# Performance work log

Measured on AMD Instinct MI355X. Metric: run time of the kernel, lower is better.

The kernel has to match this reference:

```python
import jax, jax.numpy as jnp
import numpy as np

N = 100000          # nodes
E = 1600000         # edges (before self-loops)
F_IN = 256          # num_node_features
F_MID = F_IN // 2   # conv1 out = 128
HID = 128           # hidden_channels
OUT = 64            # num_label_features
G = 128             # num graphs in batch
NEG_SLOPE = 0.2


def setup_inputs() -> dict:
    key = jax.random.key(0)
    ks = jax.random.split(key, 16)
    s = 0.05
    return {
        "x": jax.random.normal(ks[0], (N, F_IN), dtype=jnp.float32),
        "edge_index": jax.random.randint(ks[1], (2, E), 0, N, dtype=jnp.int64),
        "batch": jnp.sort(jax.random.randint(ks[2], (N,), 0, G, dtype=jnp.int64)),
        # GATConv 1 (heads=1)
        "W1": jax.random.normal(ks[3], (F_IN, F_MID), jnp.float32) * s,
        "a1_src": jax.random.normal(ks[4], (F_MID,), jnp.float32) * s,
        "a1_dst": jax.random.normal(ks[5], (F_MID,), jnp.float32) * s,
        "b1": jnp.zeros((F_MID,), jnp.float32),
        # GATConv 2
        "W2": jax.random.normal(ks[6], (F_MID, HID), jnp.float32) * s,
        "a2_src": jax.random.normal(ks[7], (HID,), jnp.float32) * s,
        "a2_dst": jax.random.normal(ks[8], (HID,), jnp.float32) * s,
        "b2": jnp.zeros((HID,), jnp.float32),
        # GlobalAttention gate nn
        "gate_W": jax.random.normal(ks[9], (HID, 1), jnp.float32) * s,
        "gate_b": jnp.zeros((1,), jnp.float32),
        # final linear
        "lin_W": jax.random.normal(ks[10], (HID, OUT), jnp.float32) * s,
        "lin_b": jnp.zeros((OUT,), jnp.float32),
    }


def _gat_conv(x, edge_index, W, a_src, a_dst, bias):
    """PyG GATConv, heads=1, add_self_loops=True, negative_slope=0.2."""
    n = x.shape[0]
    h = x @ W                                   # [N, F]
    loop = jnp.arange(n, dtype=edge_index.dtype)
    src = jnp.concatenate([edge_index[0], loop])  # message sources j
    dst = jnp.concatenate([edge_index[1], loop])  # aggregation targets i
    # per-node attention logits, gathered per-edge
    al = (h @ a_src)[src] + (h @ a_dst)[dst]    # [E+N]
    al = jax.nn.leaky_relu(al, NEG_SLOPE)
    # segment softmax over incoming edges of each dst node
    m = jax.ops.segment_max(al, dst, num_segments=n)
    e = jnp.exp(al - m[dst])
    s = jax.ops.segment_sum(e, dst, num_segments=n)
    coef = e / (s[dst] + 1e-16)
    out = jax.ops.segment_sum(h[src] * coef[:, None], dst, num_segments=n)
    return out + bias


def reference(x, edge_index, batch, W1, a1_src, a1_dst, b1,
              W2, a2_src, a2_dst, b2, gate_W, gate_b, lin_W, lin_b):
    h = _gat_conv(x, edge_index, W1, a1_src, a1_dst, b1)
    h = jax.nn.relu(h)
    h = _gat_conv(h, edge_index, W2, a2_src, a2_dst, b2)
    # GlobalAttention pooling: segment softmax of gate over batch ids
    gate = (h @ gate_W + gate_b)[:, 0]          # [N]
    gm = jax.ops.segment_max(gate, batch, num_segments=G)
    ge = jnp.exp(gate - gm[batch])
    gs = jax.ops.segment_sum(ge, batch, num_segments=G)
    attn = ge / (gs[batch] + 1e-16)
    pooled = jax.ops.segment_sum(h * attn[:, None], batch, num_segments=G)  # [G, HID]
    pooled = jax.nn.relu(pooled)
    # dropout p=0.5 is identity at inference
    return pooled @ lin_W + lin_b               # [G, OUT]
```

## Files before the change

kernel.cpp:

```cpp
#include <hip/hip_runtime.h>
#include <hip/hip_bf16.h>
#include <math.h>

#define NNODES 100000
#define NEDGES 1600000
#define EN     1700000
#define F_IN   256
#define F_MID  128
#define HID    128
#define NG     128
#define NOUT   64
#define SCAN_CHUNK 2048
#define NCHUNK ((NNODES + SCAN_CHUNK - 1) / SCAN_CHUNK)

__global__ __launch_bounds__(256) void k_init(int* deg, float* gs, float* pooled) {
    int i = blockIdx.x * 256 + threadIdx.x;
    if (i < NNODES) deg[i] = 1;
    if (i < NG) gs[i] = 0.f;
    if (i < NG * HID) pooled[i] = 0.f;
}

__global__ __launch_bounds__(256) void k_count(const int* __restrict__ ei, int* deg) {
    int e = blockIdx.x * 256 + threadIdx.x;
    if (e >= NEDGES) return;
    atomicAdd(&deg[ei[NEDGES + e]], 1);
}

__global__ __launch_bounds__(256) void k_scan_chunk(const int* __restrict__ deg,
                                                    int* rowptr, int* part) {
    __shared__ int sums[256];
    int c = blockIdx.x, t = threadIdx.x;
    int base = c * SCAN_CHUNK;
    int v[8]; int s = 0;
#pragma unroll
    for (int i = 0; i < 8; i++) {
        int idx = base + t * 8 + i;
        v[i] = (idx < NNODES) ? deg[idx] : 0;
        s += v[i];
    }
    sums[t] = s;
    __syncthreads();
    for (int off = 1; off < 256; off <<= 1) {
        int x = (t >= off) ? sums[t - off] : 0;
        __syncthreads();
        sums[t] += x;
        __syncthreads();
    }
    int run = (t == 0) ? 0 : sums[t - 1];
#pragma unroll
    for (int i = 0; i < 8; i++) {
        int idx = base + t * 8 + i;
        if (idx < NNODES) rowptr[idx] = run;
        run += v[i];
    }
    if (t == 255) part[c] = sums[255];
}

__global__ void k_scan_part(int* part, int nc) {
    if (threadIdx.x == 0) {
        int run = 0;
        for (int c = 0; c < nc; c++) { int v = part[c]; part[c] = run; run += v; }
    }
}

__global__ __launch_bounds__(256) void k_scan_add(int* rowptr, int* cursor,
                                                  const int* __restrict__ part) {
    int i = blockIdx.x * 256 + threadIdx.x;
    if (i >= NNODES) return;
    int v = rowptr[i] + part[i >> 11];
    rowptr[i] = v;
    cursor[i] = v;
}

__global__ __launch_bounds__(256) void k_fill(const int* __restrict__ ei,
                                              int* cursor, int* srcs) {
    int e = blockIdx.x * 256 + threadIdx.x;
    if (e >= EN) return;
    int src, dst;
    if (e < NEDGES) { src = ei[e]; dst = ei[NEDGES + e]; }
    else            { src = dst = e - NEDGES; }
    int pos = atomicAdd(&cursor[dst], 1);
    srcs[pos] = src;
}

template <int K>
__global__ __launch_bounds__(256) void k_gemm(const float* __restrict__ A,
                                              const float* __restrict__ B,
                                              float* __restrict__ C, int M) {
    __shared__ float As[16][128];
    __shared__ float Bs[16][128];
    int bm = blockIdx.x * 128;
    int tid = threadIdx.x;
    int tx = tid & 15, ty = tid >> 4;
    float acc[8][8] = {};
    for (int k0 = 0; k0 < K; k0 += 16) {
#pragma unroll
        for (int q = tid; q < 512; q += 256) {
            int m = q >> 2, kq = (q & 3) << 2;
            int row = bm + m;
            float4 v = make_float4(0.f, 0.f, 0.f, 0.f);
            if (row < M) v = *(const float4*)(A + (size_t)row * K + k0 + kq);
            As[kq + 0][m] = v.x; As[kq + 1][m] = v.y;
            As[kq + 2][m] = v.z; As[kq + 3][m] = v.w;
        }
#pragma unroll
        for (int q = tid; q < 512; q += 256) {
            int kk = q >> 5, n4 = (q & 31) << 2;
            *(float4*)(&Bs[kk][n4]) = *(const float4*)(B + (size_t)(k0 + kk) * 128 + n4);
        }
        __syncthreads();
#pragma unroll
        for (int kk = 0; kk < 16; kk++) {
            float a[8], b[8];
            *(float4*)(a)     = *(float4*)(&As[kk][ty * 8]);
            *(float4*)(a + 4) = *(float4*)(&As[kk][ty * 8 + 4]);
            *(float4*)(b)     = *(float4*)(&Bs[kk][tx * 8]);
            *(float4*)(b + 4) = *(float4*)(&Bs[kk][tx * 8 + 4]);
#pragma unroll
            for (int i = 0; i < 8; i++)
#pragma unroll
                for (int j = 0; j < 8; j++)
                    acc[i][j] = fmaf(a[i], b[j], acc[i][j]);
        }
        __syncthreads();
    }
#pragma unroll
    for (int i = 0; i < 8; i++) {
        int row = bm + ty * 8 + i;
        if (row < M) {
            float4* o = (float4*)(C + (size_t)row * 128 + tx * 8);
            o[0] = make_float4(acc[i][0], acc[i][1], acc[i][2], acc[i][3]);
            o[1] = make_float4(acc[i][4], acc[i][5], acc[i][6], acc[i][7]);
        }
    }
}

__global__ __launch_bounds__(256) void k_dots(const float* __restrict__ h,
                                              const float* __restrict__ asrc,
                                              const float* __restrict__ adst,
                                              float* as_, float* ad_) {
    int wid = (blockIdx.x * 256 + threadIdx.x) >> 6;
    int lane = threadIdx.x & 63;
    if (wid >= NNODES) return;
    float2 v   = ((const float2*)(h + (size_t)wid * 128))[lane];
    float2 as2 = ((const float2*)asrc)[lane];
    float2 ad2 = ((const float2*)adst)[lane];
    float s = v.x * as2.x + v.y * as2.y;
    float d = v.x * ad2.x + v.y * ad2.y;
#pragma unroll
    for (int off = 32; off; off >>= 1) {
        s += __shfl_xor(s, off);
        d += __shfl_xor(d, off);
    }
    if (lane == 0) { as_[wid] = s; ad_[wid] = d; }
}

template <bool RELU, bool GATE>
__global__ __launch_bounds__(256) void k_agg(
    const float* __restrict__ h, const float* __restrict__ as_,
    const float* __restrict__ ad_, const int* __restrict__ rowptr,
    const int* __restrict__ rowend, const int* __restrict__ srcs,
    const float* __restrict__ bias, float* __restrict__ out,
    const float* __restrict__ gateW, const float* __restrict__ gateB,
    float* __restrict__ gatev, float* __restrict__ gs,
    const int* __restrict__ batch) {
    int wid = (blockIdx.x * 256 + threadIdx.x) >> 6;
    int lane = threadIdx.x & 63;
    if (wid >= NNODES) return;
    int row = rowptr[wid];
    int dg = rowend[wid] - row;
    float adn = ad_[wid];
    const float2* __restrict__ h2 = (const float2*)h;

    float ssum = 0.f;
    float2 a0 = {0.f, 0.f}, a1 = {0.f, 0.f}, a2 = {0.f, 0.f}, a3 = {0.f, 0.f};
    float2 a4 = {0.f, 0.f}, a5 = {0.f, 0.f}, a6 = {0.f, 0.f}, a7 = {0.f, 0.f};

    for (int base = 0; base < dg; base += 64) {
        int k = base + lane;
        float ev = 0.f; int sk = 0;
        if (k < dg) {
            sk = srcs[row + k];
            float al = as_[sk] + adn;
            al = (al > 0.f) ? al : 0.2f * al;
            ev = __expf(al);
            ssum += ev;
        }
        int rem = dg - base; if (rem > 64) rem = 64;
        int kk = 0;
        for (; kk + 8 <= rem; kk += 8) {
            int   s0 = __shfl(sk, kk + 0), s1 = __shfl(sk, kk + 1);
            int   s2 = __shfl(sk, kk + 2), s3 = __shfl(sk, kk + 3);
            int   s4 = __shfl(sk, kk + 4), s5 = __shfl(sk, kk + 5);
            int   s6 = __shfl(sk, kk + 6), s7 = __shfl(sk, kk + 7);
            float e0 = __shfl(ev, kk + 0), e1 = __shfl(ev, kk + 1);
            float e2 = __shfl(ev, kk + 2), e3 = __shfl(ev, kk + 3);
            float e4 = __shfl(ev, kk + 4), e5 = __shfl(ev, kk + 5);
            float e6 = __shfl(ev, kk + 6), e7 = __shfl(ev, kk + 7);
            float2 v0 = h2[(size_t)s0 * 64 + lane];
            float2 v1 = h2[(size_t)s1 * 64 + lane];
            float2 v2 = h2[(size_t)s2 * 64 + lane];
            float2 v3 = h2[(size_t)s3 * 64 + lane];
            float2 v4 = h2[(size_t)s4 * 64 + lane];
            float2 v5 = h2[(size_t)s5 * 64 + lane];
            float2 v6 = h2[(size_t)s6 * 64 + lane];
            float2 v7 = h2[(size_t)s7 * 64 + lane];
            a0.x = fmaf(e0, v0.x, a0.x); a0.y = fmaf(e0, v0.y, a0.y);
            a1.x = fmaf(e1, v1.x, a1.x); a1.y = fmaf(e1, v1.y, a1.y);
            a2.x = fmaf(e2, v2.x, a2.x); a2.y = fmaf(e2, v2.y, a2.y);
            a3.x = fmaf(e3, v3.x, a3.x); a3.y = fmaf(e3, v3.y, a3.y);
            a4.x = fmaf(e4, v4.x, a4.x); a4.y = fmaf(e4, v4.y, a4.y);
            a5.x = fmaf(e5, v5.x, a5.x); a5.y = fmaf(e5, v5.y, a5.y);
            a6.x = fmaf(e6, v6.x, a6.x); a6.y = fmaf(e6, v6.y, a6.y);
            a7.x = fmaf(e7, v7.x, a7.x); a7.y = fmaf(e7, v7.y, a7.y);
        }
        for (; kk + 2 <= rem; kk += 2) {
            int   s0 = __shfl(sk, kk + 0), s1 = __shfl(sk, kk + 1);
            float e0 = __shfl(ev, kk + 0), e1 = __shfl(ev, kk + 1);
            float2 v0 = h2[(size_t)s0 * 64 + lane];
            float2 v1 = h2[(size_t)s1 * 64 + lane];
            a0.x = fmaf(e0, v0.x, a0.x); a0.y = fmaf(e0, v0.y, a0.y);
            a1.x = fmaf(e1, v1.x, a1.x); a1.y = fmaf(e1, v1.y, a1.y);
        }
        if (kk < rem) {
            int   s0 = __shfl(sk, kk);
            float e0 = __shfl(ev, kk);
            float2 v0 = h2[(size_t)s0 * 64 + lane];
            a0.x = fmaf(e0, v0.x, a0.x); a0.y = fmaf(e0, v0.y, a0.y);
        }
    }
    float2 acc;
    acc.x = ((a0.x + a1.x) + (a2.x + a3.x)) + ((a4.x + a5.x) + (a6.x + a7.x));
    acc.y = ((a0.y + a1.y) + (a2.y + a3.y)) + ((a4.y + a5.y) + (a6.y + a7.y));
#pragma unroll
    for (int off = 32; off; off >>= 1) ssum += __shfl_xor(ssum, off);
    float inv = 1.f / (ssum + 1e-16f);
    float2 b2v = ((const float2*)bias)[lane];
    float o0 = acc.x * inv + b2v.x;
    float o1 = acc.y * inv + b2v.y;
    if (RELU) { o0 = fmaxf(o0, 0.f); o1 = fmaxf(o1, 0.f); }
    ((float2*)(out + (size_t)wid * 128))[lane] = make_float2(o0, o1);
    if (GATE) {
        float2 gw = ((const float2*)gateW)[lane];
        float g = o0 * gw.x + o1 * gw.y;
#pragma unroll
        for (int off = 32; off; off >>= 1) g += __shfl_xor(g, off);
        if (lane == 0) {
            float ge = __expf(g + gateB[0]);
            gatev[wid] = ge;
            atomicAdd(&gs[batch[wid]], ge);
        }
    }
}

__global__ __launch_bounds__(128) void k_pool(const float* __restrict__ h,
                                              const float* __restrict__ gatev,
                                              const float* __restrict__ gs,
                                              const int* __restrict__ batch,
                                              float* pooled) {
    int t = threadIdx.x;
    int chunk = (NNODES + gridDim.x - 1) / gridDim.x;
    int s0 = blockIdx.x * chunk;
    int s1 = s0 + chunk; if (s1 > NNODES) s1 = NNODES;
    if (s0 >= s1) return;
    int curg = batch[s0];
    float invs = 1.f / (gs[curg] + 1e-16f);
    float acc = 0.f;
    for (int i = s0; i < s1; i++) {
        int g = batch[i];
        if (g != curg) {
            atomicAdd(&pooled[curg * 128 + t], acc);
            acc = 0.f; curg = g;
            invs = 1.f / (gs[g] + 1e-16f);
        }
        acc += h[(size_t)i * 128 + t] * (gatev[i] * invs);
    }
    atomicAdd(&pooled[curg * 128 + t], acc);
}

__global__ __launch_bounds__(64) void k_final(const float* __restrict__ pooled,
                                              const float* __restrict__ linW,
                                              const float* __restrict__ linb,
                                              float* __restrict__ out) {
    __shared__ float rowv[128];
    int g = blockIdx.x, t = threadIdx.x;
    rowv[t]      = fmaxf(pooled[g * 128 + t], 0.f);
    rowv[t + 64] = fmaxf(pooled[g * 128 + 64 + t], 0.f);
    __syncthreads();
    float acc = linb[t];
#pragma unroll 8
    for (int k = 0; k < 128; k++) acc = fmaf(rowv[k], linW[k * 64 + t], acc);
    out[g * 64 + t] = acc;
}

extern "C" void kernel_launch(void* const* d_in, const int* in_sizes, int n_in,
                              void* d_out, int out_size, void* d_ws, size_t ws_size,
                              hipStream_t stream) {
    const float* x     = (const float*)d_in[0];
    const int*   ei    = (const int*)d_in[1];
    const int*   batch = (const int*)d_in[2];
    const float* W1    = (const float*)d_in[3];
    const float* a1s   = (const float*)d_in[4];
    const float* a1d   = (const float*)d_in[5];
    const float* b1    = (const float*)d_in[6];
    const float* W2    = (const float*)d_in[7];
    const float* a2s   = (const float*)d_in[8];
    const float* a2d   = (const float*)d_in[9];
    const float* b2    = (const float*)d_in[10];
    const float* gateW = (const float*)d_in[11];
    const float* gateB = (const float*)d_in[12];
    const float* linW  = (const float*)d_in[13];
    const float* linb  = (const float*)d_in[14];
    float* out = (float*)d_out;

    char* p = (char*)d_ws;
    auto alloc = [&](size_t bytes) -> void* {
        void* r = (void*)p;
        p += (bytes + 255) & ~(size_t)255;
        return r;
    };
    float* bufA   = (float*)alloc((size_t)NNODES * 128 * 4);
    float* bufB   = (float*)alloc((size_t)NNODES * 128 * 4);
    float* as_    = (float*)alloc((size_t)NNODES * 4);
    float* ad_    = (float*)alloc((size_t)NNODES * 4);
    float* gatev  = (float*)alloc((size_t)NNODES * 4);
    int*   deg    = (int*)alloc((size_t)NNODES * 4);
    int*   rowptr = (int*)alloc((size_t)NNODES * 4);
    int*   cursor = (int*)alloc((size_t)NNODES * 4);
    int*   srcs   = (int*)alloc((size_t)EN * 4);
    int*   part   = (int*)alloc(64 * 4);
    float* gs     = (float*)alloc(NG * 4);
    float* pooled = (float*)alloc((size_t)NG * HID * 4);

    const int gN   = (NNODES + 255) / 256;
    const int gE   = (NEDGES + 255) / 256;
    const int gEN  = (EN + 255) / 256;
    const int gW   = (NNODES + 3) / 4;

    k_init<<<gN, 256, 0, stream>>>(deg, gs, pooled);
    k_count<<<gE, 256, 0, stream>>>(ei, deg);
    k_scan_chunk<<<NCHUNK, 256, 0, stream>>>(deg, rowptr, part);
    k_scan_part<<<1, 64, 0, stream>>>(part, NCHUNK);
    k_scan_add<<<gN, 256, 0, stream>>>(rowptr, cursor, part);
    k_fill<<<gEN, 256, 0, stream>>>(ei, cursor, srcs);

    k_gemm<256><<<(NNODES + 127) / 128, 256, 0, stream>>>(x, W1, bufA, NNODES);
    k_dots<<<gW, 256, 0, stream>>>(bufA, a1s, a1d, as_, ad_);
    k_agg<true, false><<<gW, 256, 0, stream>>>(bufA, as_, ad_, rowptr, cursor, srcs,
                                               b1, bufB, nullptr, nullptr, nullptr,
                                               nullptr, nullptr);
    k_gemm<128><<<(NNODES + 127) / 128, 256, 0, stream>>>(bufB, W2, bufA, NNODES);
    k_dots<<<gW, 256, 0, stream>>>(bufA, a2s, a2d, as_, ad_);
    k_agg<false, true><<<gW, 256, 0, stream>>>(bufA, as_, ad_, rowptr, cursor, srcs,
                                               b2, bufB, gateW, gateB, gatev, gs,
                                               batch);
    k_pool<<<512, 128, 0, stream>>>(bufB, gatev, gs, batch, pooled);
    k_final<<<NG, 64, 0, stream>>>(pooled, linW, linb, out);
}
```

Baseline: 1.130 ms.

## Store intermediate node features in bf16 to halve gather traffic

The GEMM outputs and the first aggregation output are now stored as packed bf16 instead of fp32. The dots, aggregation and second GEMM read and unpack bf16, and all math stays in fp32. The main aim is to halve the bytes moved by the random per-edge row gathers in the aggregation kernels, which dominate memory traffic. The cost is reduced precision of the intermediate features, which could push the result past the accuracy tolerance.

```diff
diff --git a/kernel.cpp b/kernel.cpp
--- a/kernel.cpp
+++ b/kernel.cpp
@@ -13,6 +13,16 @@
 #define SCAN_CHUNK 2048
 #define NCHUNK ((NNODES + SCAN_CHUNK - 1) / SCAN_CHUNK)
 
+typedef unsigned int  u32;
+typedef unsigned short u16;
+
+__device__ __forceinline__ float bfl(u32 u) { return __uint_as_float(u << 16); }
+__device__ __forceinline__ float bfh(u32 u) { return __uint_as_float(u & 0xFFFF0000u); }
+__device__ __forceinline__ u32 f2bf(float f) {
+    u32 x = __float_as_uint(f);
+    return (x + 0x7FFFu + ((x >> 16) & 1u)) >> 16;
+}
+
 __global__ __launch_bounds__(256) void k_init(int* deg, float* gs, float* pooled) {
     int i = blockIdx.x * 256 + threadIdx.x;
     if (i < NNODES) deg[i] = 1;
@@ -83,10 +93,10 @@
     srcs[pos] = src;
 }
 
-template <int K>
-__global__ __launch_bounds__(256) void k_gemm(const float* __restrict__ A,
+template <int K, bool ABF>
+__global__ __launch_bounds__(256) void k_gemm(const void* __restrict__ Av,
                                               const float* __restrict__ B,
-                                              float* __restrict__ C, int M) {
+                                              u16* __restrict__ C, int M) {
     __shared__ float As[16][128];
     __shared__ float Bs[16][128];
     int bm = blockIdx.x * 128;
@@ -98,10 +108,19 @@
         for (int q = tid; q < 512; q += 256) {
             int m = q >> 2, kq = (q & 3) << 2;
             int row = bm + m;
-            float4 v = make_float4(0.f, 0.f, 0.f, 0.f);
-            if (row < M) v = *(const float4*)(A + (size_t)row * K + k0 + kq);
-            As[kq + 0][m] = v.x; As[kq + 1][m] = v.y;
-            As[kq + 2][m] = v.z; As[kq + 3][m] = v.w;
+            if (ABF) {
+                const u16* A = (const u16*)Av;
+                uint2 v = make_uint2(0u, 0u);
+                if (row < M) v = *(const uint2*)(A + (size_t)row * K + k0 + kq);
+                As[kq + 0][m] = bfl(v.x); As[kq + 1][m] = bfh(v.x);
+                As[kq + 2][m] = bfl(v.y); As[kq + 3][m] = bfh(v.y);
+            } else {
+                const float* A = (const float*)Av;
+                float4 v = make_float4(0.f, 0.f, 0.f, 0.f);
+                if (row < M) v = *(const float4*)(A + (size_t)row * K + k0 + kq);
+                As[kq + 0][m] = v.x; As[kq + 1][m] = v.y;
+                As[kq + 2][m] = v.z; As[kq + 3][m] = v.w;
+            }
         }
 #pragma unroll
         for (int q = tid; q < 512; q += 256) {
@@ -128,25 +147,29 @@
     for (int i = 0; i < 8; i++) {
         int row = bm + ty * 8 + i;
         if (row < M) {
-            float4* o = (float4*)(C + (size_t)row * 128 + tx * 8);
-            o[0] = make_float4(acc[i][0], acc[i][1], acc[i][2], acc[i][3]);
-            o[1] = make_float4(acc[i][4], acc[i][5], acc[i][6], acc[i][7]);
-        }
-    }
-}
-
-__global__ __launch_bounds__(256) void k_dots(const float* __restrict__ h,
+            uint4 o;
+            o.x = f2bf(acc[i][0]) | (f2bf(acc[i][1]) << 16);
+            o.y = f2bf(acc[i][2]) | (f2bf(acc[i][3]) << 16);
+            o.z = f2bf(acc[i][4]) | (f2bf(acc[i][5]) << 16);
+            o.w = f2bf(acc[i][6]) | (f2bf(acc[i][7]) << 16);
+            *(uint4*)(C + (size_t)row * 128 + tx * 8) = o;
+        }
+    }
+}
+
+__global__ __launch_bounds__(256) void k_dots(const u32* __restrict__ h,
                                               const float* __restrict__ asrc,
                                               const float* __restrict__ adst,
                                               float* as_, float* ad_) {
     int wid = (blockIdx.x * 256 + threadIdx.x) >> 6;
     int lane = threadIdx.x & 63;
     if (wid >= NNODES) return;
-    float2 v   = ((const float2*)(h + (size_t)wid * 128))[lane];
+    u32 u = h[(size_t)wid * 64 + lane];
+    float vx = bfl(u), vy = bfh(u);
     float2 as2 = ((const float2*)asrc)[lane];
     float2 ad2 = ((const float2*)adst)[lane];
-    float s = v.x * as2.x + v.y * as2.y;
-    float d = v.x * ad2.x + v.y * ad2.y;
+    float s = vx * as2.x + vy * as2.y;
+    float d = vx * ad2.x + vy * ad2.y;
 #pragma unroll
     for (int off = 32; off; off >>= 1) {
         s += __shfl_xor(s, off);
@@ -155,12 +178,12 @@
     if (lane == 0) { as_[wid] = s; ad_[wid] = d; }
 }
 
-template <bool RELU, bool GATE>
+template <bool RELU, bool GATE, bool OUTBF>
 __global__ __launch_bounds__(256) void k_agg(
-    const float* __restrict__ h, const float* __restrict__ as_,
+    const u32* __restrict__ h, const float* __restrict__ as_,
     const float* __restrict__ ad_, const int* __restrict__ rowptr,
     const int* __restrict__ rowend, const int* __restrict__ srcs,
-    const float* __restrict__ bias, float* __restrict__ out,
+    const float* __restrict__ bias, void* __restrict__ outv,
     const float* __restrict__ gateW, const float* __restrict__ gateB,
     float* __restrict__ gatev, float* __restrict__ gs,
     const int* __restrict__ batch) {
@@ -170,7 +193,6 @@
     int row = rowptr[wid];
     int dg = rowend[wid] - row;
     float adn = ad_[wid];
-    const float2* __restrict__ h2 = (const float2*)h;
 
     float ssum = 0.f;
     float2 a0 = {0.f, 0.f}, a1 = {0.f, 0.f}, a2 = {0.f, 0.f}, a3 = {0.f, 0.f};
@@ -197,36 +219,36 @@
             float e2 = __shfl(ev, kk + 2), e3 = __shfl(ev, kk + 3);
             float e4 = __shfl(ev, kk + 4), e5 = __shfl(ev, kk + 5);
             float e6 = __shfl(ev, kk + 6), e7 = __shfl(ev, kk + 7);
-            float2 v0 = h2[(size_t)s0 * 64 + lane];
-            float2 v1 = h2[(size_t)s1 * 64 + lane];
-            float2 v2 = h2[(size_t)s2 * 64 + lane];
-            float2 v3 = h2[(size_t)s3 * 64 + lane];
-            float2 v4 = h2[(size_t)s4 * 64 + lane];
-            float2 v5 = h2[(size_t)s5 * 64 + lane];
-            float2 v6 = h2[(size_t)s6 * 64 + lane];
-            float2 v7 = h2[(size_t)s7 * 64 + lane];
-            a0.x = fmaf(e0, v0.x, a0.x); a0.y = fmaf(e0, v0.y, a0.y);
-            a1.x = fmaf(e1, v1.x, a1.x); a1.y = fmaf(e1, v1.y, a1.y);
-            a2.x = fmaf(e2, v2.x, a2.x); a2.y = fmaf(e2, v2.y, a2.y);
-            a3.x = fmaf(e3, v3.x, a3.x); a3.y = fmaf(e3, v3.y, a3.y);
-            a4.x = fmaf(e4, v4.x, a4.x); a4.y = fmaf(e4, v4.y, a4.y);
-            a5.x = fmaf(e5, v5.x, a5.x); a5.y = fmaf(e5, v5.y, a5.y);
-            a6.x = fmaf(e6, v6.x, a6.x); a6.y = fmaf(e6, v6.y, a6.y);
-            a7.x = fmaf(e7, v7.x, a7.x); a7.y = fmaf(e7, v7.y, a7.y);
+            u32 u0 = h[(size_t)s0 * 64 + lane];
+            u32 u1 = h[(size_t)s1 * 64 + lane];
+            u32 u2 = h[(size_t)s2 * 64 + lane];
+            u32 u3 = h[(size_t)s3 * 64 + lane];
+            u32 u4 = h[(size_t)s4 * 64 + lane];
+            u32 u5 = h[(size_t)s5 * 64 + lane];
+            u32 u6 = h[(size_t)s6 * 64 + lane];
+            u32 u7 = h[(size_t)s7 * 64 + lane];
+            a0.x = fmaf(e0, bfl(u0), a0.x); a0.y = fmaf(e0, bfh(u0), a0.y);
+            a1.x = fmaf(e1, bfl(u1), a1.x); a1.y = fmaf(e1, bfh(u1), a1.y);
+            a2.x = fmaf(e2, bfl(u2), a2.x); a2.y = fmaf(e2, bfh(u2), a2.y);
+            a3.x = fmaf(e3, bfl(u3), a3.x); a3.y = fmaf(e3, bfh(u3), a3.y);
+            a4.x = fmaf(e4, bfl(u4), a4.x); a4.y = fmaf(e4, bfh(u4), a4.y);
+            a5.x = fmaf(e5, bfl(u5), a5.x); a5.y = fmaf(e5, bfh(u5), a5.y);
+            a6.x = fmaf(e6, bfl(u6), a6.x); a6.y = fmaf(e6, bfh(u6), a6.y);
+            a7.x = fmaf(e7, bfl(u7), a7.x); a7.y = fmaf(e7, bfh(u7), a7.y);
         }
         for (; kk + 2 <= rem; kk += 2) {
             int   s0 = __shfl(sk, kk + 0), s1 = __shfl(sk, kk + 1);
             float e0 = __shfl(ev, kk + 0), e1 = __shfl(ev, kk + 1);
-            float2 v0 = h2[(size_t)s0 * 64 + lane];
-            float2 v1 = h2[(size_t)s1 * 64 + lane];
-            a0.x = fmaf(e0, v0.x, a0.x); a0.y = fmaf(e0, v0.y, a0.y);
-            a1.x = fmaf(e1, v1.x, a1.x); a1.y = fmaf(e1, v1.y, a1.y);
+            u32 u0 = h[(size_t)s0 * 64 + lane];
+            u32 u1 = h[(size_t)s1 * 64 + lane];
+            a0.x = fmaf(e0, bfl(u0), a0.x); a0.y = fmaf(e0, bfh(u0), a0.y);
+            a1.x = fmaf(e1, bfl(u1), a1.x); a1.y = fmaf(e1, bfh(u1), a1.y);
         }
         if (kk < rem) {
             int   s0 = __shfl(sk, kk);
             float e0 = __shfl(ev, kk);
-            float2 v0 = h2[(size_t)s0 * 64 + lane];
-            a0.x = fmaf(e0, v0.x, a0.x); a0.y = fmaf(e0, v0.y, a0.y);
+            u32 u0 = h[(size_t)s0 * 64 + lane];
+            a0.x = fmaf(e0, bfl(u0), a0.x); a0.y = fmaf(e0, bfh(u0), a0.y);
         }
     }
     float2 acc;
@@ -239,7 +261,11 @@
     float o0 = acc.x * inv + b2v.x;
     float o1 = acc.y * inv + b2v.y;
     if (RELU) { o0 = fmaxf(o0, 0.f); o1 = fmaxf(o1, 0.f); }
-    ((float2*)(out + (size_t)wid * 128))[lane] = make_float2(o0, o1);
+    if (OUTBF) {
+        ((u32*)outv)[(size_t)wid * 64 + lane] = f2bf(o0) | (f2bf(o1) << 16);
+    } else {
+        ((float2*)((float*)outv + (size_t)wid * 128))[lane] = make_float2(o0, o1);
+    }
     if (GATE) {
         float2 gw = ((const float2*)gateW)[lane];
         float g = o0 * gw.x + o1 * gw.y;
@@ -319,8 +345,9 @@
         p += (bytes + 255) & ~(size_t)255;
         return r;
     };
-    float* bufA   = (float*)alloc((size_t)NNODES * 128 * 4);
-    float* bufB   = (float*)alloc((size_t)NNODES * 128 * 4);
+    u16*   hb     = (u16*)alloc((size_t)NNODES * 128 * 2);
+    u16*   h1a    = (u16*)alloc((size_t)NNODES * 128 * 2);
+    float* bufF   = (float*)alloc((size_t)NNODES * 128 * 4);
     float* as_    = (float*)alloc((size_t)NNODES * 4);
     float* ad_    = (float*)alloc((size_t)NNODES * 4);
     float* gatev  = (float*)alloc((size_t)NNODES * 4);
@@ -344,16 +371,17 @@
     k_scan_add<<<gN, 256, 0, stream>>>(rowptr, cursor, part);
     k_fill<<<gEN, 256, 0, stream>>>(ei, cursor, srcs);
 
-    k_gemm<256><<<(NNODES + 127) / 128, 256, 0, stream>>>(x, W1, bufA, NNODES);
-    k_dots<<<gW, 256, 0, stream>>>(bufA, a1s, a1d, as_, ad_);
-    k_agg<true, false><<<gW, 256, 0, stream>>>(bufA, as_, ad_, rowptr, cursor, srcs,
-                                               b1, bufB, nullptr, nullptr, nullptr,
-                                               nullptr, nullptr);
-    k_gemm<128><<<(NNODES + 127) / 128, 256, 0, stream>>>(bufB, W2, bufA, NNODES);
-    k_dots<<<gW, 256, 0, stream>>>(bufA, a2s, a2d, as_, ad_);
-    k_agg<false, true><<<gW, 256, 0, stream>>>(bufA, as_, ad_, rowptr, cursor, srcs,
-                                               b2, bufB, gateW, gateB, gatev, gs,
-                                               batch);
-    k_pool<<<512, 128, 0, stream>>>(bufB, gatev, gs, batch, pooled);
+    k_gemm<256, false><<<(NNODES + 127) / 128, 256, 0, stream>>>(x, W1, hb, NNODES);
+    k_dots<<<gW, 256, 0, stream>>>((const u32*)hb, a1s, a1d, as_, ad_);
+    k_agg<true, false, true><<<gW, 256, 0, stream>>>((const u32*)hb, as_, ad_,
+                                                     rowptr, cursor, srcs, b1, h1a,
+                                                     nullptr, nullptr, nullptr,
+                                                     nullptr, nullptr);
+    k_gemm<128, true><<<(NNODES + 127) / 128, 256, 0, stream>>>(h1a, W2, hb, NNODES);
+    k_dots<<<gW, 256, 0, stream>>>((const u32*)hb, a2s, a2d, as_, ad_);
+    k_agg<false, true, false><<<gW, 256, 0, stream>>>((const u32*)hb, as_, ad_,
+                                                      rowptr, cursor, srcs, b2, bufF,
+                                                      gateW, gateB, gatev, gs, batch);
+    k_pool<<<512, 128, 0, stream>>>(bufF, gatev, gs, batch, pooled);
     k_final<<<NG, 64, 0, stream>>>(pooled, linW, linb, out);
 }
```

New measurement: 1.141 ms. No clear change (+0.9%).
